# Kernel tuning notes

Measured on AMD Instinct MI355X. Metric: run time of the kernel, lower is better.

Reference implementation:

```python
import jax, jax.numpy as jnp
import numpy as np

H = 64        # hidden_size
G = 64        # global_hidden_size
VOCAB = 128   # VOCAB_SIZE
NUM_OPS = 20
DEPTH = 12    # complete binary tree: 2**DEPTH - 1 nodes
B = 128       # batch of trees
TEMP = 3.0    # self.temperature


def setup_inputs() -> dict:
    key = jax.random.key(0)
    ks = jax.random.split(key, 16)
    s = 0.05
    N = 2 ** DEPTH - 1
    inp = {
        "x_idx": jax.random.randint(ks[0], (B, N), 0, VOCAB, dtype=jnp.int32),
        "validity_mask": jnp.ones((NUM_OPS,), jnp.float32),
        # binary tree-LSTM (blstm): x one-hot -> gates [i, f_a, f_b, o, u]
        "Wx": jax.random.normal(ks[1], (VOCAB, 5 * H), jnp.float32) * s,
        "Ua": jax.random.normal(ks[2], (H, 5 * H), jnp.float32) * s,
        "Ub": jax.random.normal(ks[3], (H, 5 * H), jnp.float32) * s,
        "b_tree": jnp.zeros((5 * H,), jnp.float32),
        # global nn.LSTM (1 layer), gate order i,f,g,o
        "W_ih": jax.random.normal(ks[4], (H, 4 * G), jnp.float32) * s,
        "W_hh": jax.random.normal(ks[5], (G, 4 * G), jnp.float32) * s,
        "b_lstm": jnp.zeros((4 * G,), jnp.float32),
        # FFN on root hidden
        "W1": jax.random.normal(ks[6], (H, H), jnp.float32) * s,
        "b1": jnp.zeros((H,), jnp.float32),
        "W2": jax.random.normal(ks[7], (H, H), jnp.float32) * s,
        "b2": jnp.zeros((H,), jnp.float32),
        # actor head on [hidden ; global_hidden]
        "actor_W": jax.random.normal(ks[8], (H + G, NUM_OPS), jnp.float32) * s,
        "actor_b": jnp.zeros((NUM_OPS,), jnp.float32),
    }
    return inp


def _tree_lstm_sweep(x_idx, Wx, Ua, Ub, b_tree):
    """Bottom-up binary tree-LSTM over a complete binary tree.
    Node i's children sit at flat positions 2i+1, 2i+2 (level layout)."""
    h_prev = c_prev = None
    for d in range(DEPTH - 1, -1, -1):
        n = 2 ** d
        off = n - 1
        # memory-bound gather of gate pre-activations: [B, n, 5H]
        z = Wx[x_idx[:, off:off + n]] + b_tree
        if h_prev is not None:
            h_a, h_b = h_prev[:, 0::2], h_prev[:, 1::2]
            c_a, c_b = c_prev[:, 0::2], c_prev[:, 1::2]
            z = z + jnp.einsum("bnh,hg->bng", h_a, Ua) + jnp.einsum("bnh,hg->bng", h_b, Ub)
        i, fa, fb, o, u = jnp.split(z, 5, axis=-1)
        c = jax.nn.sigmoid(i) * jnp.tanh(u)
        if h_prev is not None:
            c = c + jax.nn.sigmoid(fa) * c_a + jax.nn.sigmoid(fb) * c_b
        h = jax.nn.sigmoid(o) * jnp.tanh(c)
        h_prev, c_prev = h, c
    return h_prev[:, 0]  # root hidden [B, H]


def reference(x_idx, validity_mask, Wx, Ua, Ub, b_tree, W_ih, W_hh, b_lstm,
              W1, b1, W2, b2, actor_W, actor_b):
    h_root = _tree_lstm_sweep(x_idx, Wx, Ua, Ub, b_tree)
    # internal op 1: apply_ffn then apply_global_lstm
    f = jnp.maximum(h_root @ W1 + b1, 0.0) @ W2 + b2          # FFN [B, H]
    h0 = jnp.zeros((f.shape[0], G), f.dtype)
    g = f @ W_ih + h0 @ W_hh + b_lstm                          # one LSTM step
    i, fg, gg, o = jnp.split(g, 4, axis=-1)                    # torch order i,f,g,o
    c_g = jax.nn.sigmoid(i) * jnp.tanh(gg)                     # c0 = 0
    h_g = jax.nn.sigmoid(o) * jnp.tanh(c_g)                    # [B, G]
    # external actor with validity-masked weights (as in policy())
    feats = jnp.concatenate([f, h_g], axis=-1)                 # [B, H+G]
    logits = jnp.log(validity_mask) + feats @ (actor_W * validity_mask) + actor_b * validity_mask
    return jax.nn.softmax(logits / TEMP, axis=-1)              # [B, NUM_OPS]
```

## Files before the change

### kernel.cpp

```cpp
#include <hip/hip_runtime.h>


typedef unsigned short u16;
typedef unsigned int   u32;
typedef __attribute__((ext_vector_type(8))) short  short8;
typedef __attribute__((ext_vector_type(4))) float  floatx4;

__device__ __forceinline__ float fsig(float x) {
    return __fdividef(1.0f, 1.0f + __expf(-x));
}
__device__ __forceinline__ float ftanh(float x) {
    return 1.0f - __fdividef(2.0f, __expf(2.0f * x) + 1.0f);
}
__device__ __forceinline__ u16 f2bfa(float x) {
    return (u16)((__float_as_uint(x) + 0x8000u) >> 16);
}
__device__ __forceinline__ float bflo(u32 cc) { return __uint_as_float(cc << 16); }
__device__ __forceinline__ float bfhi(u32 cc) { return __uint_as_float(cc & 0xFFFF0000u); }

#define HS 72

__global__ void precompute_kernel(
    const float* __restrict__ Wx, const float* __restrict__ b_tree,
    const float* __restrict__ Ua, const float* __restrict__ Ub,
    float4* __restrict__ WpA, float* __restrict__ WpU,
    float4* __restrict__ TaA, float2* __restrict__ TaUC,
    float4* __restrict__ TbA, float2* __restrict__ TbUC,
    u16* __restrict__ Uswz)
{
    int v = blockIdx.x;
    int t = threadIdx.x;
    __shared__ float sz[320], sta[320], stb[320], sh[64], sc[64];
    float z = Wx[v * 320 + t] + b_tree[t];
    sz[t] = z;
    {
        int f = v * 320 + t;
        int j = f & 7, lane = (f >> 3) & 63, tk = f >> 9;
        int nt = tk % 20, kc = tk / 20;
        int k = kc * 32 + (lane >> 4) * 8 + j;
        int nn = nt * 16 + (lane & 15);
        float uval = (k < 64) ? Ua[k * 320 + nn] : Ub[(k - 64) * 320 + nn];
        Uswz[f] = (u16)((__float_as_uint(uval) + 0x7FFFu +
                         ((__float_as_uint(uval) >> 16) & 1u)) >> 16);
    }
    __syncthreads();
    if (t < 64) {
        float c = fsig(sz[t]) * ftanh(sz[256 + t]);
        float h = fsig(sz[192 + t]) * ftanh(c);
        sc[t] = c; sh[t] = h;
    }
    __syncthreads();
    float ta = 0.f, tb = 0.f;
    #pragma unroll 8
    for (int k = 0; k < 64; ++k) {
        ta += sh[k] * Ua[k * 320 + t];
        tb += sh[k] * Ub[k * 320 + t];
    }
    sta[t] = ta; stb[t] = tb;
    __syncthreads();
    if (t < 64) {
        int o = (v << 6) + t;
        WpA[o]  = make_float4(sz[t],  sz[64 + t],  sz[128 + t],  sz[192 + t]);
        WpU[o]  = sz[256 + t];
        TaA[o]  = make_float4(sta[t], sta[64 + t], sta[128 + t], sta[192 + t]);
        TaUC[o] = make_float2(sta[256 + t], sc[t]);
        TbA[o]  = make_float4(stb[t], stb[64 + t], stb[128 + t], stb[192 + t]);
        TbUC[o] = make_float2(stb[256 + t], sc[t]);
    }
}

template<int NT, int MODE>
__device__ __forceinline__ void sweep_level(
    const u16* hsrc, const u16* cps,
    u16* hdst, u16* cpd, u16* hg, u16* cg, float* hroot,
    const short8 Bfrag[4][5],
    const float4* __restrict__ WpA, const float* __restrict__ WpU,
    const int* __restrict__ xb, int loff, int lbase0, int node0,
    int lane15, int quad, int wv)
{
    floatx4 acc[NT][5];
    #pragma unroll
    for (int mt = 0; mt < NT; ++mt)
        #pragma unroll
        for (int g = 0; g < 5; ++g) acc[mt][g] = (floatx4){0.f, 0.f, 0.f, 0.f};

    #pragma unroll
    for (int mt = 0; mt < NT; ++mt) {
        #pragma unroll
        for (int kc = 0; kc < 4; ++kc) {
            int child = 2 * (lbase0 + mt * 16 + lane15) + (kc >> 1);
            short8 a = *(const short8*)(hsrc + child * HS + (kc & 1) * 32 + quad * 8);
            #pragma unroll
            for (int g = 0; g < 5; ++g)
                acc[mt][g] = __builtin_amdgcn_mfma_f32_16x16x32_bf16(
                    a, Bfrag[kc][g], acc[mt][g], 0, 0, 0);
        }
    }
    int hh = wv * 16 + lane15;
    #pragma unroll
    for (int mt = 0; mt < NT; ++mt) {
        #pragma unroll
        for (int r = 0; r < 4; ++r) {
            int lrow = lbase0 + mt * 16 + quad * 4 + r;
            int node = node0 + mt * 16 + quad * 4 + r;
            int id = xb[loff + node];
            float4 wg = WpA[(id << 6) + hh];
            float  wu = WpU[(id << 6) + hh];
            u32 cc = *(const u32*)(cps + lrow * 128 + hh * 2);
            float zi  = acc[mt][0][r] + wg.x;
            float zfa = acc[mt][1][r] + wg.y;
            float zfb = acc[mt][2][r] + wg.z;
            float zo  = acc[mt][3][r] + wg.w;
            float zu  = acc[mt][4][r] + wu;
            float c = fsig(zi) * ftanh(zu) + fsig(zfa) * bflo(cc) + fsig(zfb) * bfhi(cc);
            float h = fsig(zo) * ftanh(c);
            if (MODE == 0) {
                hdst[lrow * HS + hh] = f2bfa(h);
                cpd[(lrow >> 1) * 128 + hh * 2 + (lrow & 1)] = f2bfa(c);
            }
            if (MODE == 1) {
                hg[node * 64 + hh] = f2bfa(h);
                cg[(node >> 1) * 128 + hh * 2 + (node & 1)] = f2bfa(c);
            }
            if (MODE == 2) {
                if (lrow == 0) hroot[hh] = h;
            }
        }
    }
}

__device__ __forceinline__ void load_bfrags(short8 Bfrag[4][5],
                                            const u16* __restrict__ Uswz,
                                            int wv, int lane)
{
    #pragma unroll
    for (int kc = 0; kc < 4; ++kc)
        #pragma unroll
        for (int g = 0; g < 5; ++g) {
            int nt = g * 4 + wv;
            Bfrag[kc][g] = *(const short8*)(Uswz + ((kc * 20 + nt) * 64 + lane) * 8);
        }
}

__global__ __launch_bounds__(256, 2) void sweepA_kernel(
    const int* __restrict__ x_idx,
    const float4* __restrict__ WpA, const float* __restrict__ WpU,
    const float4* __restrict__ TaA, const float2* __restrict__ TaUC,
    const float4* __restrict__ TbA, const float2* __restrict__ TbUC,
    const u16* __restrict__ Uswz,
    u16* __restrict__ h7, u16* __restrict__ c7)
{
    __shared__ u16 hA[128 * HS];
    __shared__ u16 cA[64 * 128];
    __shared__ u16 hB[64 * HS];
    __shared__ u16 cB[32 * 128];
    int t = threadIdx.x, lane = t & 63, wv = t >> 6;
    int lane15 = lane & 15, quad = lane >> 4;
    int b = blockIdx.x >> 3, st = blockIdx.x & 7;
    const int* xb = x_idx + b * 4095;

    short8 Bfrag[4][5];
    load_bfrags(Bfrag, Uswz, wv, lane);

    #pragma unroll 2
    for (int rr = 0; rr < 32; ++rr) {
        int rl = wv * 32 + rr;
        int i = st * 128 + rl;
        int id  = xb[1023 + i];
        int ida = xb[2047 + 2 * i];
        int idb = xb[2048 + 2 * i];
        float4 wg  = WpA[(id  << 6) + lane];
        float  wu  = WpU[(id  << 6) + lane];
        float4 tga = TaA[(ida << 6) + lane];
        float2 tua = TaUC[(ida << 6) + lane];
        float4 tgb = TbA[(idb << 6) + lane];
        float2 tub = TbUC[(idb << 6) + lane];
        float zi  = wg.x + tga.x + tgb.x;
        float zfa = wg.y + tga.y + tgb.y;
        float zfb = wg.z + tga.z + tgb.z;
        float zo  = wg.w + tga.w + tgb.w;
        float zu  = wu   + tua.x + tub.x;
        float c = fsig(zi) * ftanh(zu) + fsig(zfa) * tua.y + fsig(zfb) * tub.y;
        float h = fsig(zo) * ftanh(c);
        hA[rl * HS + lane] = f2bfa(h);
        cA[(rl >> 1) * 128 + lane * 2 + (rl & 1)] = f2bfa(c);
    }
    __syncthreads();
    sweep_level<2, 0>(hA, cA, hB, cB, nullptr, nullptr, nullptr, Bfrag, WpA, WpU,
                      xb, 511, 0,  st * 64,      lane15, quad, wv);
    sweep_level<2, 0>(hA, cA, hB, cB, nullptr, nullptr, nullptr, Bfrag, WpA, WpU,
                      xb, 511, 32, st * 64 + 32, lane15, quad, wv);
    __syncthreads();
    sweep_level<2, 0>(hB, cB, hA, cA, nullptr, nullptr, nullptr, Bfrag, WpA, WpU,
                      xb, 255, 0, st * 32, lane15, quad, wv);
    __syncthreads();
    sweep_level<1, 1>(hA, cA, nullptr, nullptr,
                      h7 + (size_t)b * 8192, c7 + (size_t)b * 8192, nullptr,
                      Bfrag, WpA, WpU, xb, 127, 0, st * 16, lane15, quad, wv);
}

__global__ __launch_bounds__(256, 2) void sweepB_kernel(
    const int* __restrict__ x_idx,
    const float4* __restrict__ WpA, const float* __restrict__ WpU,
    const u16* __restrict__ Uswz,
    const u16* __restrict__ h7, const u16* __restrict__ c7,
    const float* __restrict__ W1, const float* __restrict__ b1,
    const float* __restrict__ W2, const float* __restrict__ b2,
    const float* __restrict__ W_ih, const float* __restrict__ b_lstm,
    const float* __restrict__ actor_W, const float* __restrict__ actor_b,
    const float* __restrict__ vm, float* __restrict__ out)
{
    __shared__ u16 hA[128 * HS];
    __shared__ u16 cA[64 * 128];
    __shared__ u16 hB[64 * HS];
    __shared__ u16 cB[32 * 128];
    __shared__ float hroot[64];
    int t = threadIdx.x, lane = t & 63, wv = t >> 6;
    int lane15 = lane & 15, quad = lane >> 4;
    int b = blockIdx.x;
    const int* xb = x_idx + b * 4095;
    const u16* h7b = h7 + (size_t)b * 8192;
    const u16* c7b = c7 + (size_t)b * 8192;

    short8 Bfrag[4][5];
    load_bfrags(Bfrag, Uswz, wv, lane);

    for (int idx = t; idx < 4096; idx += 256) {
        int r = idx >> 5, p2 = (idx & 31) * 2;
        *(u32*)&hA[r * HS + p2] = *(const u32*)&h7b[r * 64 + p2];
        *(u32*)&cA[idx * 2] = *(const u32*)&c7b[idx * 2];
    }
    __syncthreads();
    sweep_level<2, 0>(hA, cA, hB, cB, nullptr, nullptr, nullptr, Bfrag, WpA, WpU,
                      xb, 63, 0, 0, lane15, quad, wv);
    sweep_level<2, 0>(hA, cA, hB, cB, nullptr, nullptr, nullptr, Bfrag, WpA, WpU,
                      xb, 63, 32, 32, lane15, quad, wv);
    __syncthreads();
    sweep_level<2, 0>(hB, cB, hA, cA, nullptr, nullptr, nullptr, Bfrag, WpA, WpU,
                      xb, 31, 0, 0, lane15, quad, wv);
    __syncthreads();
    sweep_level<1, 0>(hA, cA, hB, cB, nullptr, nullptr, nullptr, Bfrag, WpA, WpU,
                      xb, 15, 0, 0, lane15, quad, wv);
    __syncthreads();
    sweep_level<1, 0>(hB, cB, hA, cA, nullptr, nullptr, nullptr, Bfrag, WpA, WpU,
                      xb, 7, 0, 0, lane15, quad, wv);
    __syncthreads();
    sweep_level<1, 0>(hA, cA, hB, cB, nullptr, nullptr, nullptr, Bfrag, WpA, WpU,
                      xb, 3, 0, 0, lane15, quad, wv);
    __syncthreads();
    sweep_level<1, 0>(hB, cB, hA, cA, nullptr, nullptr, nullptr, Bfrag, WpA, WpU,
                      xb, 1, 0, 0, lane15, quad, wv);
    __syncthreads();
    sweep_level<1, 2>(hA, cA, nullptr, nullptr, nullptr, nullptr, hroot,
                      Bfrag, WpA, WpU, xb, 0, 0, 0, lane15, quad, wv);
    __syncthreads();

    if (wv == 0) {
        float a = b1[lane];
        #pragma unroll 8
        for (int k = 0; k < 64; ++k) a += hroot[k] * W1[k * 64 + lane];
        float r1 = fmaxf(a, 0.f);
        float f = b2[lane];
        #pragma unroll 8
        for (int k = 0; k < 64; ++k) f += __shfl(r1, k) * W2[k * 64 + lane];
        float gi = b_lstm[lane], gg = b_lstm[128 + lane], go = b_lstm[192 + lane];
        #pragma unroll 8
        for (int k = 0; k < 64; ++k) {
            float fk = __shfl(f, k);
            gi += fk * W_ih[k * 256 + lane];
            gg += fk * W_ih[k * 256 + 128 + lane];
            go += fk * W_ih[k * 256 + 192 + lane];
        }
        float cg = fsig(gi) * ftanh(gg);
        float hg = fsig(go) * ftanh(cg);
        int tt = (lane < 20) ? lane : 19;
        float dot = 0.f;
        #pragma unroll 8
        for (int k = 0; k < 64; ++k) {
            float fk = __shfl(f, k), hk = __shfl(hg, k);
            dot += fk * actor_W[k * 20 + tt] + hk * actor_W[(64 + k) * 20 + tt];
        }
        float m = vm[tt];
        float lg = logf(m) + dot * m + actor_b[tt] * m;
        float mx = -1e30f;
        #pragma unroll
        for (int j = 0; j < 20; ++j) mx = fmaxf(mx, __shfl(lg, j));
        float s = 0.f;
        #pragma unroll
        for (int j = 0; j < 20; ++j) s += __expf((__shfl(lg, j) - mx) * (1.0f / 3.0f));
        if (lane < 20) out[b * 20 + lane] = __expf((lg - mx) * (1.0f / 3.0f)) / s;
    }
}

extern "C" void kernel_launch(void* const* d_in, const int* in_sizes, int n_in,
                              void* d_out, int out_size, void* d_ws, size_t ws_size,
                              hipStream_t stream)
{
    const int*   x_idx   = (const int*)d_in[0];
    const float* vm      = (const float*)d_in[1];
    const float* Wx      = (const float*)d_in[2];
    const float* Ua      = (const float*)d_in[3];
    const float* Ub      = (const float*)d_in[4];
    const float* b_tree  = (const float*)d_in[5];
    const float* W_ih    = (const float*)d_in[6];
    const float* b_lstm  = (const float*)d_in[8];
    const float* W1      = (const float*)d_in[9];
    const float* b1      = (const float*)d_in[10];
    const float* W2      = (const float*)d_in[11];
    const float* b2      = (const float*)d_in[12];
    const float* actor_W = (const float*)d_in[13];
    const float* actor_b = (const float*)d_in[14];
    float* out = (float*)d_out;

    char* ws = (char*)d_ws;
    float4* WpA  = (float4*)ws;            ws += 128 * 64 * 16;
    float4* TaA  = (float4*)ws;            ws += 128 * 64 * 16;
    float4* TbA  = (float4*)ws;            ws += 128 * 64 * 16;
    float2* TaUC = (float2*)ws;            ws += 128 * 64 * 8;
    float2* TbUC = (float2*)ws;            ws += 128 * 64 * 8;
    float*  WpU  = (float*)ws;             ws += 128 * 64 * 4;
    u16*    h7   = (u16*)ws;               ws += 128 * 8192 * 2;
    u16*    c7   = (u16*)ws;               ws += 128 * 8192 * 2;
    u16*    Uswz = (u16*)ws;               ws += 128 * 320 * 2;

    precompute_kernel<<<128, 320, 0, stream>>>(Wx, b_tree, Ua, Ub,
                                               WpA, WpU, TaA, TaUC, TbA, TbUC, Uswz);
    sweepA_kernel<<<1024, 256, 0, stream>>>(x_idx, WpA, WpU, TaA, TaUC,
                                            TbA, TbUC, Uswz, h7, c7);
    sweepB_kernel<<<128, 256, 0, stream>>>(x_idx, WpA, WpU, Uswz, h7, c7,
                                           W1, b1, W2, b2, W_ih, b_lstm,
                                           actor_W, actor_b, vm, out);
}
```

Baseline: 182.0 us.

## Fuse two sweep kernels via per-tree atomic last-block-finishes pattern

Merges the two sweep kernels into one launch of 2048 blocks. Each block handles a 1/16 slice of a tree's lower levels, and the last block to arrive (tracked by an atomic counter) reads the level-7 state directly from global memory and finishes the top levels plus the head. It also packs the gate tables into 32-byte records, stages node ids in shared memory, widens the shared row stride, and raises the occupancy hint. The aim is to remove a kernel boundary and the serial 128-block tail's copy-in. The cost is an extra memset, atomics, and a tail that still runs on only 128 blocks.

```diff
diff --git a/kernel.cpp b/kernel.cpp
--- a/kernel.cpp
+++ b/kernel.cpp
@@ -18,14 +18,12 @@
 __device__ __forceinline__ float bflo(u32 cc) { return __uint_as_float(cc << 16); }
 __device__ __forceinline__ float bfhi(u32 cc) { return __uint_as_float(cc & 0xFFFF0000u); }
 
-#define HS 72
+#define HS 76
 
 __global__ void precompute_kernel(
     const float* __restrict__ Wx, const float* __restrict__ b_tree,
     const float* __restrict__ Ua, const float* __restrict__ Ub,
-    float4* __restrict__ WpA, float* __restrict__ WpU,
-    float4* __restrict__ TaA, float2* __restrict__ TaUC,
-    float4* __restrict__ TbA, float2* __restrict__ TbUC,
+    float* __restrict__ Wrec, float* __restrict__ Tarec, float* __restrict__ Tbrec,
     u16* __restrict__ Uswz)
 {
     int v = blockIdx.x;
@@ -59,23 +57,25 @@
     sta[t] = ta; stb[t] = tb;
     __syncthreads();
     if (t < 64) {
-        int o = (v << 6) + t;
-        WpA[o]  = make_float4(sz[t],  sz[64 + t],  sz[128 + t],  sz[192 + t]);
-        WpU[o]  = sz[256 + t];
-        TaA[o]  = make_float4(sta[t], sta[64 + t], sta[128 + t], sta[192 + t]);
-        TaUC[o] = make_float2(sta[256 + t], sc[t]);
-        TbA[o]  = make_float4(stb[t], stb[64 + t], stb[128 + t], stb[192 + t]);
-        TbUC[o] = make_float2(stb[256 + t], sc[t]);
-    }
-}
-
-template<int NT, int MODE>
+        float* w  = Wrec  + (((size_t)v << 6) + t) * 8;
+        float* pa = Tarec + (((size_t)v << 6) + t) * 8;
+        float* pb = Tbrec + (((size_t)v << 6) + t) * 8;
+        *(float4*)w        = make_float4(sz[t], sz[64 + t], sz[128 + t], sz[192 + t]);
+        *(float4*)(w + 4)  = make_float4(sz[256 + t], 0.f, 0.f, 0.f);
+        *(float4*)pa       = make_float4(sta[t], sta[64 + t], sta[128 + t], sta[192 + t]);
+        *(float4*)(pa + 4) = make_float4(sta[256 + t], sc[t], 0.f, 0.f);
+        *(float4*)pb       = make_float4(stb[t], stb[64 + t], stb[128 + t], stb[192 + t]);
+        *(float4*)(pb + 4) = make_float4(stb[256 + t], sc[t], 0.f, 0.f);
+    }
+}
+
+template<int NT, int MODE, int GSRC>
 __device__ __forceinline__ void sweep_level(
-    const u16* hsrc, const u16* cps,
-    u16* hdst, u16* cpd, u16* hg, u16* cg, float* hroot,
+    const u16* hsrc, const u32* csrc,
+    u16* hdst, u16* cdst, u16* hg, u16* cg, float* hroot,
     const short8 Bfrag[4][5],
-    const float4* __restrict__ WpA, const float* __restrict__ WpU,
-    const int* __restrict__ xb, int loff, int lbase0, int node0,
+    const float* __restrict__ Wrec,
+    const int* ids, int lbase, int node0g, int nvalid,
     int lane15, int quad, int wv)
 {
     floatx4 acc[NT][5];
@@ -88,8 +88,10 @@
     for (int mt = 0; mt < NT; ++mt) {
         #pragma unroll
         for (int kc = 0; kc < 4; ++kc) {
-            int child = 2 * (lbase0 + mt * 16 + lane15) + (kc >> 1);
-            short8 a = *(const short8*)(hsrc + child * HS + (kc & 1) * 32 + quad * 8);
+            int child = 2 * (lbase + mt * 16 + lane15) + (kc >> 1);
+            const u16* ap = GSRC ? (hsrc + child * 64 + (kc & 1) * 32 + quad * 8)
+                                 : (hsrc + child * HS + (kc & 1) * 32 + quad * 8);
+            short8 a = *(const short8*)ap;
             #pragma unroll
             for (int g = 0; g < 5; ++g)
                 acc[mt][g] = __builtin_amdgcn_mfma_f32_16x16x32_bf16(
@@ -101,12 +103,12 @@
     for (int mt = 0; mt < NT; ++mt) {
         #pragma unroll
         for (int r = 0; r < 4; ++r) {
-            int lrow = lbase0 + mt * 16 + quad * 4 + r;
-            int node = node0 + mt * 16 + quad * 4 + r;
-            int id = xb[loff + node];
-            float4 wg = WpA[(id << 6) + hh];
-            float  wu = WpU[(id << 6) + hh];
-            u32 cc = *(const u32*)(cps + lrow * 128 + hh * 2);
+            int lrow = lbase + mt * 16 + quad * 4 + r;
+            int id = ids[lrow];
+            const float* w = Wrec + (((size_t)id << 6) + hh) * 8;
+            float4 wg = *(const float4*)w;
+            float  wu = w[4];
+            u32 cc = csrc[lrow * 64 + hh];
             float zi  = acc[mt][0][r] + wg.x;
             float zfa = acc[mt][1][r] + wg.y;
             float zfb = acc[mt][2][r] + wg.z;
@@ -116,11 +118,14 @@
             float h = fsig(zo) * ftanh(c);
             if (MODE == 0) {
                 hdst[lrow * HS + hh] = f2bfa(h);
-                cpd[(lrow >> 1) * 128 + hh * 2 + (lrow & 1)] = f2bfa(c);
+                cdst[(lrow >> 1) * 128 + hh * 2 + (lrow & 1)] = f2bfa(c);
             }
             if (MODE == 1) {
-                hg[node * 64 + hh] = f2bfa(h);
-                cg[(node >> 1) * 128 + hh * 2 + (node & 1)] = f2bfa(c);
+                if (lrow < nvalid) {
+                    int node = node0g + lrow;
+                    hg[node * 64 + hh] = f2bfa(h);
+                    cg[(node >> 1) * 128 + hh * 2 + (node & 1)] = f2bfa(c);
+                }
             }
             if (MODE == 2) {
                 if (lrow == 0) hroot[hh] = h;
@@ -142,117 +147,108 @@
         }
 }
 
-__global__ __launch_bounds__(256, 2) void sweepA_kernel(
+__global__ __launch_bounds__(256, 3) void sweep_kernel(
     const int* __restrict__ x_idx,
-    const float4* __restrict__ WpA, const float* __restrict__ WpU,
-    const float4* __restrict__ TaA, const float2* __restrict__ TaUC,
-    const float4* __restrict__ TbA, const float2* __restrict__ TbUC,
-    const u16* __restrict__ Uswz,
-    u16* __restrict__ h7, u16* __restrict__ c7)
-{
-    __shared__ u16 hA[128 * HS];
-    __shared__ u16 cA[64 * 128];
-    __shared__ u16 hB[64 * HS];
-    __shared__ u16 cB[32 * 128];
-    int t = threadIdx.x, lane = t & 63, wv = t >> 6;
-    int lane15 = lane & 15, quad = lane >> 4;
-    int b = blockIdx.x >> 3, st = blockIdx.x & 7;
-    const int* xb = x_idx + b * 4095;
-
-    short8 Bfrag[4][5];
-    load_bfrags(Bfrag, Uswz, wv, lane);
-
-    #pragma unroll 2
-    for (int rr = 0; rr < 32; ++rr) {
-        int rl = wv * 32 + rr;
-        int i = st * 128 + rl;
-        int id  = xb[1023 + i];
-        int ida = xb[2047 + 2 * i];
-        int idb = xb[2048 + 2 * i];
-        float4 wg  = WpA[(id  << 6) + lane];
-        float  wu  = WpU[(id  << 6) + lane];
-        float4 tga = TaA[(ida << 6) + lane];
-        float2 tua = TaUC[(ida << 6) + lane];
-        float4 tgb = TbA[(idb << 6) + lane];
-        float2 tub = TbUC[(idb << 6) + lane];
-        float zi  = wg.x + tga.x + tgb.x;
-        float zfa = wg.y + tga.y + tgb.y;
-        float zfb = wg.z + tga.z + tgb.z;
-        float zo  = wg.w + tga.w + tgb.w;
-        float zu  = wu   + tua.x + tub.x;
-        float c = fsig(zi) * ftanh(zu) + fsig(zfa) * tua.y + fsig(zfb) * tub.y;
-        float h = fsig(zo) * ftanh(c);
-        hA[rl * HS + lane] = f2bfa(h);
-        cA[(rl >> 1) * 128 + lane * 2 + (rl & 1)] = f2bfa(c);
-    }
-    __syncthreads();
-    sweep_level<2, 0>(hA, cA, hB, cB, nullptr, nullptr, nullptr, Bfrag, WpA, WpU,
-                      xb, 511, 0,  st * 64,      lane15, quad, wv);
-    sweep_level<2, 0>(hA, cA, hB, cB, nullptr, nullptr, nullptr, Bfrag, WpA, WpU,
-                      xb, 511, 32, st * 64 + 32, lane15, quad, wv);
-    __syncthreads();
-    sweep_level<2, 0>(hB, cB, hA, cA, nullptr, nullptr, nullptr, Bfrag, WpA, WpU,
-                      xb, 255, 0, st * 32, lane15, quad, wv);
-    __syncthreads();
-    sweep_level<1, 1>(hA, cA, nullptr, nullptr,
-                      h7 + (size_t)b * 8192, c7 + (size_t)b * 8192, nullptr,
-                      Bfrag, WpA, WpU, xb, 127, 0, st * 16, lane15, quad, wv);
-}
-
-__global__ __launch_bounds__(256, 2) void sweepB_kernel(
-    const int* __restrict__ x_idx,
-    const float4* __restrict__ WpA, const float* __restrict__ WpU,
-    const u16* __restrict__ Uswz,
-    const u16* __restrict__ h7, const u16* __restrict__ c7,
+    const float* __restrict__ Wrec, const float* __restrict__ Tarec,
+    const float* __restrict__ Tbrec, const u16* __restrict__ Uswz,
+    u16* __restrict__ h7, u16* __restrict__ c7, int* __restrict__ cnt,
     const float* __restrict__ W1, const float* __restrict__ b1,
     const float* __restrict__ W2, const float* __restrict__ b2,
     const float* __restrict__ W_ih, const float* __restrict__ b_lstm,
     const float* __restrict__ actor_W, const float* __restrict__ actor_b,
     const float* __restrict__ vm, float* __restrict__ out)
 {
-    __shared__ u16 hA[128 * HS];
-    __shared__ u16 cA[64 * 128];
-    __shared__ u16 hB[64 * HS];
-    __shared__ u16 cB[32 * 128];
+    __shared__ u16 hA[64 * HS];
+    __shared__ u16 cA[32 * 128];
+    __shared__ u16 hB[32 * HS];
+    __shared__ u16 cB[16 * 128];
+    __shared__ int sIds[256];
     __shared__ float hroot[64];
+    __shared__ int go;
     int t = threadIdx.x, lane = t & 63, wv = t >> 6;
     int lane15 = lane & 15, quad = lane >> 4;
-    int b = blockIdx.x;
+    int b = blockIdx.x >> 4, st = blockIdx.x & 15;
     const int* xb = x_idx + b * 4095;
-    const u16* h7b = h7 + (size_t)b * 8192;
-    const u16* c7b = c7 + (size_t)b * 8192;
-
+    u16* h7b = h7 + (size_t)b * 8192;
+    u16* c7b = c7 + (size_t)b * 8192;
+
+    if      (t < 64)  sIds[t] = xb[1023 + st * 64 + t];
+    else if (t < 192) sIds[t] = xb[2047 + st * 128 + (t - 64)];
+    else if (t < 224) sIds[t] = xb[511 + st * 32 + (t - 192)];
+    else if (t < 240) sIds[t] = xb[255 + st * 16 + (t - 224)];
+    else if (t < 248) sIds[t] = xb[127 + st * 8 + (t - 240)];
+    else              sIds[t] = 0;
+    __syncthreads();
+
+    #pragma unroll 4
+    for (int rr = 0; rr < 16; ++rr) {
+        int rl = wv * 16 + rr;
+        int id  = sIds[rl];
+        int ida = sIds[64 + 2 * rl];
+        int idb = sIds[65 + 2 * rl];
+        const float* w  = Wrec  + (((size_t)id  << 6) + lane) * 8;
+        const float* pa = Tarec + (((size_t)ida << 6) + lane) * 8;
+        const float* pb = Tbrec + (((size_t)idb << 6) + lane) * 8;
+        float4 wg = *(const float4*)w;   float  wu = w[4];
+        float4 ga = *(const float4*)pa;  float2 ua = *(const float2*)(pa + 4);
+        float4 gb = *(const float4*)pb;  float2 ub = *(const float2*)(pb + 4);
+        float zi  = wg.x + ga.x + gb.x;
+        float zfa = wg.y + ga.y + gb.y;
+        float zfb = wg.z + ga.z + gb.z;
+        float zo  = wg.w + ga.w + gb.w;
+        float zu  = wu   + ua.x + ub.x;
+        float c = fsig(zi) * ftanh(zu) + fsig(zfa) * ua.y + fsig(zfb) * ub.y;
+        float h = fsig(zo) * ftanh(c);
+        hA[rl * HS + lane] = f2bfa(h);
+        cA[(rl >> 1) * 128 + lane * 2 + (rl & 1)] = f2bfa(c);
+    }
     short8 Bfrag[4][5];
     load_bfrags(Bfrag, Uswz, wv, lane);
-
-    for (int idx = t; idx < 4096; idx += 256) {
-        int r = idx >> 5, p2 = (idx & 31) * 2;
-        *(u32*)&hA[r * HS + p2] = *(const u32*)&h7b[r * 64 + p2];
-        *(u32*)&cA[idx * 2] = *(const u32*)&c7b[idx * 2];
-    }
-    __syncthreads();
-    sweep_level<2, 0>(hA, cA, hB, cB, nullptr, nullptr, nullptr, Bfrag, WpA, WpU,
-                      xb, 63, 0, 0, lane15, quad, wv);
-    sweep_level<2, 0>(hA, cA, hB, cB, nullptr, nullptr, nullptr, Bfrag, WpA, WpU,
-                      xb, 63, 32, 32, lane15, quad, wv);
-    __syncthreads();
-    sweep_level<2, 0>(hB, cB, hA, cA, nullptr, nullptr, nullptr, Bfrag, WpA, WpU,
-                      xb, 31, 0, 0, lane15, quad, wv);
-    __syncthreads();
-    sweep_level<1, 0>(hA, cA, hB, cB, nullptr, nullptr, nullptr, Bfrag, WpA, WpU,
-                      xb, 15, 0, 0, lane15, quad, wv);
-    __syncthreads();
-    sweep_level<1, 0>(hB, cB, hA, cA, nullptr, nullptr, nullptr, Bfrag, WpA, WpU,
-                      xb, 7, 0, 0, lane15, quad, wv);
-    __syncthreads();
-    sweep_level<1, 0>(hA, cA, hB, cB, nullptr, nullptr, nullptr, Bfrag, WpA, WpU,
-                      xb, 3, 0, 0, lane15, quad, wv);
-    __syncthreads();
-    sweep_level<1, 0>(hB, cB, hA, cA, nullptr, nullptr, nullptr, Bfrag, WpA, WpU,
-                      xb, 1, 0, 0, lane15, quad, wv);
-    __syncthreads();
-    sweep_level<1, 2>(hA, cA, nullptr, nullptr, nullptr, nullptr, hroot,
-                      Bfrag, WpA, WpU, xb, 0, 0, 0, lane15, quad, wv);
+    __syncthreads();
+    sweep_level<2, 0, 0>(hA, (const u32*)cA, hB, cB, nullptr, nullptr, nullptr,
+                         Bfrag, Wrec, &sIds[192], 0, 0, 32, lane15, quad, wv);
+    __syncthreads();
+    sweep_level<1, 0, 0>(hB, (const u32*)cB, hA, cA, nullptr, nullptr, nullptr,
+                         Bfrag, Wrec, &sIds[224], 0, 0, 16, lane15, quad, wv);
+    __syncthreads();
+    sweep_level<1, 1, 0>(hA, (const u32*)cA, nullptr, nullptr, h7b, c7b, nullptr,
+                         Bfrag, Wrec, &sIds[240], 0, st * 8, 8, lane15, quad, wv);
+
+    __syncthreads();
+    if (t == 0) {
+        __threadfence();
+        int old = __hip_atomic_fetch_add(&cnt[b], 1, __ATOMIC_ACQ_REL,
+                                         __HIP_MEMORY_SCOPE_AGENT);
+        go = (old == 15);
+        if (old == 15) __threadfence();
+    }
+    __syncthreads();
+    if (!go) return;
+
+    if (t < 127) sIds[t] = xb[t];
+    __syncthreads();
+    sweep_level<2, 0, 1>(h7b, (const u32*)c7b, hA, cA, nullptr, nullptr, nullptr,
+                         Bfrag, Wrec, &sIds[63], 0, 0, 64, lane15, quad, wv);
+    sweep_level<2, 0, 1>(h7b, (const u32*)c7b, hA, cA, nullptr, nullptr, nullptr,
+                         Bfrag, Wrec, &sIds[63], 32, 0, 64, lane15, quad, wv);
+    __syncthreads();
+    sweep_level<2, 0, 0>(hA, (const u32*)cA, hB, cB, nullptr, nullptr, nullptr,
+                         Bfrag, Wrec, &sIds[31], 0, 0, 32, lane15, quad, wv);
+    __syncthreads();
+    sweep_level<1, 0, 0>(hB, (const u32*)cB, hA, cA, nullptr, nullptr, nullptr,
+                         Bfrag, Wrec, &sIds[15], 0, 0, 16, lane15, quad, wv);
+    __syncthreads();
+    sweep_level<1, 0, 0>(hA, (const u32*)cA, hB, cB, nullptr, nullptr, nullptr,
+                         Bfrag, Wrec, &sIds[7], 0, 0, 8, lane15, quad, wv);
+    __syncthreads();
+    sweep_level<1, 0, 0>(hB, (const u32*)cB, hA, cA, nullptr, nullptr, nullptr,
+                         Bfrag, Wrec, &sIds[3], 0, 0, 4, lane15, quad, wv);
+    __syncthreads();
+    sweep_level<1, 0, 0>(hA, (const u32*)cA, hB, cB, nullptr, nullptr, nullptr,
+                         Bfrag, Wrec, &sIds[1], 0, 0, 2, lane15, quad, wv);
+    __syncthreads();
+    sweep_level<1, 2, 0>(hB, (const u32*)cB, nullptr, nullptr, nullptr, nullptr,
+                         hroot, Bfrag, Wrec, &sIds[0], 0, 0, 1, lane15, quad, wv);
     __syncthreads();
 
     if (wv == 0) {
@@ -263,16 +259,16 @@
         float f = b2[lane];
         #pragma unroll 8
         for (int k = 0; k < 64; ++k) f += __shfl(r1, k) * W2[k * 64 + lane];
-        float gi = b_lstm[lane], gg = b_lstm[128 + lane], go = b_lstm[192 + lane];
+        float gi = b_lstm[lane], gg = b_lstm[128 + lane], go2 = b_lstm[192 + lane];
         #pragma unroll 8
         for (int k = 0; k < 64; ++k) {
             float fk = __shfl(f, k);
-            gi += fk * W_ih[k * 256 + lane];
-            gg += fk * W_ih[k * 256 + 128 + lane];
-            go += fk * W_ih[k * 256 + 192 + lane];
+            gi  += fk * W_ih[k * 256 + lane];
+            gg  += fk * W_ih[k * 256 + 128 + lane];
+            go2 += fk * W_ih[k * 256 + 192 + lane];
         }
         float cg = fsig(gi) * ftanh(gg);
-        float hg = fsig(go) * ftanh(cg);
+        float hg = fsig(go2) * ftanh(cg);
         int tt = (lane < 20) ? lane : 19;
         float dot = 0.f;
         #pragma unroll 8
@@ -313,21 +309,19 @@
     float* out = (float*)d_out;
 
     char* ws = (char*)d_ws;
-    float4* WpA  = (float4*)ws;            ws += 128 * 64 * 16;
-    float4* TaA  = (float4*)ws;            ws += 128 * 64 * 16;
-    float4* TbA  = (float4*)ws;            ws += 128 * 64 * 16;
-    float2* TaUC = (float2*)ws;            ws += 128 * 64 * 8;
-    float2* TbUC = (float2*)ws;            ws += 128 * 64 * 8;
-    float*  WpU  = (float*)ws;             ws += 128 * 64 * 4;
-    u16*    h7   = (u16*)ws;               ws += 128 * 8192 * 2;
-    u16*    c7   = (u16*)ws;               ws += 128 * 8192 * 2;
-    u16*    Uswz = (u16*)ws;               ws += 128 * 320 * 2;
-
+    float* Wrec  = (float*)ws;  ws += 128 * 64 * 8 * 4;
+    float* Tarec = (float*)ws;  ws += 128 * 64 * 8 * 4;
+    float* Tbrec = (float*)ws;  ws += 128 * 64 * 8 * 4;
+    u16*   h7    = (u16*)ws;    ws += 128 * 128 * 64 * 2;
+    u16*   c7    = (u16*)ws;    ws += 128 * 128 * 64 * 2;
+    u16*   Uswz  = (u16*)ws;    ws += 128 * 320 * 2;
+    int*   cnt   = (int*)ws;    ws += 128 * 4;
+
+    hipMemsetAsync(cnt, 0, 128 * 4, stream);
     precompute_kernel<<<128, 320, 0, stream>>>(Wx, b_tree, Ua, Ub,
-                                               WpA, WpU, TaA, TaUC, TbA, TbUC, Uswz);
-    sweepA_kernel<<<1024, 256, 0, stream>>>(x_idx, WpA, WpU, TaA, TaUC,
-                                            TbA, TbUC, Uswz, h7, c7);
-    sweepB_kernel<<<128, 256, 0, stream>>>(x_idx, WpA, WpU, Uswz, h7, c7,
+                                               Wrec, Tarec, Tbrec, Uswz);
+    sweep_kernel<<<2048, 256, 0, stream>>>(x_idx, Wrec, Tarec, Tbrec, Uswz,
+                                           h7, c7, cnt,
                                            W1, b1, W2, b2, W_ih, b_lstm,
                                            actor_W, actor_b, vm, out);
 }
```

After: 362.5 us. 1.99x slower.
